# Optimization experiments

Measured on AMD Instinct MI355X. Metric: run time of the kernel, lower is better.

The kernel has to match this reference:

```python
import jax, jax.numpy as jnp
import numpy as np
from jax import lax

D_MODEL, D_STATE, D_CONV, EXPAND = 512, 16, 4, 2
D_INNER = EXPAND * D_MODEL          # 1024
DT_RANK = (D_MODEL + 15) // 16      # 32
BATCH, SEQ = 4, 1024


def setup_inputs() -> dict:
    key = jax.random.key(0)
    ks = jax.random.split(key, 8)
    s = 0.02
    x = jax.random.normal(ks[0], (BATCH, SEQ, D_MODEL), jnp.float32)
    in_proj_w = jax.random.normal(ks[1], (2 * D_INNER, D_MODEL), jnp.float32) * s
    conv_w = jax.random.normal(ks[2], (D_INNER, 1, D_CONV), jnp.float32) * s  # depthwise
    conv_b = jnp.zeros((D_INNER,), jnp.float32)
    x_proj_w = jax.random.normal(ks[3], (DT_RANK + 2 * D_STATE, D_INNER), jnp.float32) * s
    dt_proj_w = jax.random.normal(ks[4], (D_INNER, DT_RANK), jnp.float32) * s
    dt_proj_b = jax.random.normal(ks[5], (D_INNER,), jnp.float32) * 0.1
    # Mamba S4D-real init: A = -[1..d_state] per channel, stored as log
    A_log = jnp.log(jnp.tile(jnp.arange(1, D_STATE + 1, dtype=jnp.float32)[None, :], (D_INNER, 1)))
    D = jnp.ones((D_INNER,), jnp.float32)
    out_proj_w = jax.random.normal(ks[6], (D_MODEL, D_INNER), jnp.float32) * s
    ln_w = jnp.ones((D_MODEL,), jnp.float32)
    ln_b = jnp.zeros((D_MODEL,), jnp.float32)
    return dict(x=x, in_proj_w=in_proj_w, conv_w=conv_w, conv_b=conv_b,
                x_proj_w=x_proj_w, dt_proj_w=dt_proj_w, dt_proj_b=dt_proj_b,
                A_log=A_log, D=D, out_proj_w=out_proj_w, ln_w=ln_w, ln_b=ln_b)


def _selective_scan(u, delta, A, Bm, Cm, D):
    # u, delta: (B,L,Di); A: (Di,N); Bm, Cm: (B,L,N)
    dA = jnp.exp(delta[..., None] * A)                    # (B,L,Di,N)
    dBu = (delta * u)[..., None] * Bm[:, :, None, :]      # (B,L,Di,N)
    dA_t = jnp.moveaxis(dA, 1, 0)                         # (L,B,Di,N)
    dBu_t = jnp.moveaxis(dBu, 1, 0)
    C_t = jnp.moveaxis(Cm, 1, 0)                          # (L,B,N)

    def step(h, inp):
        dA_i, dBu_i, C_i = inp
        h = dA_i * h + dBu_i                              # (B,Di,N)
        y = jnp.einsum('bdn,bn->bd', h, C_i)
        return h, y

    h0 = jnp.zeros((u.shape[0], A.shape[0], A.shape[1]), u.dtype)
    _, ys = lax.scan(step, h0, (dA_t, dBu_t, C_t))        # ys: (L,B,Di)
    return jnp.moveaxis(ys, 0, 1) + u * D                 # (B,L,Di)


def reference(x, in_proj_w, conv_w, conv_b, x_proj_w, dt_proj_w, dt_proj_b,
              A_log, D, out_proj_w, ln_w, ln_b):
    # ---- Mamba SSM ----
    xz = jnp.einsum('bld,ed->ble', x, in_proj_w)          # (B,L,2*Di)
    xs, z = jnp.split(xz, 2, axis=-1)
    # causal depthwise conv over time
    xt = jnp.moveaxis(xs, 1, 2)                           # (B,Di,L)
    xt = lax.conv_general_dilated(xt, conv_w, window_strides=(1,),
                                  padding=[(D_CONV - 1, 0)],
                                  feature_group_count=D_INNER,
                                  dimension_numbers=('NCH', 'OIH', 'NCH'))
    xt = xt + conv_b[None, :, None]
    u = jax.nn.silu(jnp.moveaxis(xt, 1, 2))               # (B,L,Di)

    x_dbl = jnp.einsum('bld,ed->ble', u, x_proj_w)        # (B,L,dt_rank+2N)
    dt = x_dbl[..., :DT_RANK]
    Bm = x_dbl[..., DT_RANK:DT_RANK + D_STATE]
    Cm = x_dbl[..., DT_RANK + D_STATE:]
    delta = jax.nn.softplus(jnp.einsum('blr,dr->bld', dt, dt_proj_w) + dt_proj_b)
    A = -jnp.exp(A_log)                                   # (Di,N)

    y = _selective_scan(u, delta, A, Bm, Cm, D)
    y = y * jax.nn.silu(z)
    ssm_out = jnp.einsum('ble,de->bld', y, out_proj_w)    # (B,L,Dm)

    # ---- residual + LayerNorm ----
    r = x + ssm_out
    mu = jnp.mean(r, axis=-1, keepdims=True)
    var = jnp.mean(jnp.square(r - mu), axis=-1, keepdims=True)
    return (r - mu) / jnp.sqrt(var + 1e-5) * ln_w + ln_b
```

## Files before the change

kernel.cpp:

```cpp
#include <hip/hip_runtime.h>
#include <hip/hip_bf16.h>
#include <math.h>

#define B_   4
#define L_   1024
#define DM   512
#define DI   1024
#define NS   16
#define XDC  64
#define BL   4096
#define G_   16
#define SEG  64
#define KS   4

typedef short bfrag __attribute__((ext_vector_type(8)));
typedef float ffrag __attribute__((ext_vector_type(4)));

__device__ __forceinline__ ushort f2bf(float v) {
    __hip_bfloat16 h = __float2bfloat16(v);
    return *(ushort*)&h;
}

__global__ __launch_bounds__(256) void cast_bf16(const float* __restrict__ in,
        ushort* __restrict__ out, int n4)
{
    int i = blockIdx.x * 256 + threadIdx.x;
    if (i >= n4) return;
    float4 v = ((const float4*)in)[i];
    ushort4 o;
    o.x = f2bf(v.x); o.y = f2bf(v.y); o.z = f2bf(v.z); o.w = f2bf(v.w);
    ((ushort4*)out)[i] = o;
}

template<int EPI>
__global__ __launch_bounds__(256) void gemm_mfma(const ushort* __restrict__ A,
        const ushort* __restrict__ B, float* __restrict__ C,
        int K, int ldc, const float* __restrict__ resid)
{
    __shared__ ushort As[128][40];
    __shared__ ushort Bs[128][40];
    const int tid = threadIdx.x;
    const int lane = tid & 63, wave = tid >> 6;
    const int wm = (wave & 1) * 64, wn = (wave >> 1) * 64;
    const int l15 = lane & 15, quad = lane >> 4;
    const int m0 = blockIdx.y * 128, n0 = blockIdx.x * 128;

    ffrag acc[4][4] = {};

    for (int k0 = 0; k0 < K; k0 += 32) {
        #pragma unroll
        for (int i = 0; i < 2; i++) {
            int chunk = tid + i * 256;
            int row = chunk >> 2, kk8 = (chunk & 3) * 8;
            *(uint4*)&As[row][kk8] = *(const uint4*)&A[(size_t)(m0 + row) * K + k0 + kk8];
            *(uint4*)&Bs[row][kk8] = *(const uint4*)&B[(size_t)(n0 + row) * K + k0 + kk8];
        }
        __syncthreads();
        bfrag af[4], bfv[4];
        #pragma unroll
        for (int i = 0; i < 4; i++) {
            af[i]  = *(const bfrag*)&As[wm + i * 16 + l15][quad * 8];
            bfv[i] = *(const bfrag*)&Bs[wn + i * 16 + l15][quad * 8];
        }
        #pragma unroll
        for (int i = 0; i < 4; i++)
            #pragma unroll
            for (int j = 0; j < 4; j++)
                acc[i][j] = __builtin_amdgcn_mfma_f32_16x16x32_bf16(af[i], bfv[j], acc[i][j], 0, 0, 0);
        __syncthreads();
    }

    #pragma unroll
    for (int i = 0; i < 4; i++) {
        #pragma unroll
        for (int j = 0; j < 4; j++) {
            int n = n0 + wn + j * 16 + l15;
            #pragma unroll
            for (int r = 0; r < 4; r++) {
                int m = m0 + wm + i * 16 + quad * 4 + r;
                float v = acc[i][j][r];
                if (EPI == 2) v += resid[(size_t)m * ldc + n];
                C[(size_t)m * ldc + n] = v;
            }
        }
    }
}

__global__ __launch_bounds__(256) void gemm_tn128(const float* __restrict__ A,
        const float* __restrict__ W, float* __restrict__ C,
        int N, int K, int lda, int ldw, int ldc,
        const float* __restrict__ bias)
{
    __shared__ float As[16][132];
    __shared__ float Ws[16][68];
    const int tid = threadIdx.x;
    const int tx = tid & 15, ty = tid >> 4;
    const int n0 = blockIdx.x * 64, m0 = blockIdx.y * 128;
    float acc[8][4] = {};

    for (int k0 = 0; k0 < K; k0 += 16) {
        #pragma unroll
        for (int i = 0; i < 2; i++) {
            int idx = tid * 2 + i;
            int r = idx >> 2, c4 = (idx & 3) * 4;
            const float4 v = *(const float4*)&A[(size_t)(m0 + r) * lda + k0 + c4];
            As[c4 + 0][r] = v.x; As[c4 + 1][r] = v.y;
            As[c4 + 2][r] = v.z; As[c4 + 3][r] = v.w;
        }
        {
            int r = tid >> 2, c4 = (tid & 3) * 4;
            const float4 v = *(const float4*)&W[(size_t)(n0 + r) * ldw + k0 + c4];
            Ws[c4 + 0][r] = v.x; Ws[c4 + 1][r] = v.y;
            Ws[c4 + 2][r] = v.z; Ws[c4 + 3][r] = v.w;
        }
        __syncthreads();
        #pragma unroll
        for (int kk = 0; kk < 16; kk++) {
            float a[8], b[4];
            #pragma unroll
            for (int i = 0; i < 8; i++) a[i] = As[kk][ty * 8 + i];
            #pragma unroll
            for (int j = 0; j < 4; j++) b[j] = Ws[kk][tx * 4 + j];
            #pragma unroll
            for (int i = 0; i < 8; i++)
                #pragma unroll
                for (int j = 0; j < 4; j++)
                    acc[i][j] = fmaf(a[i], b[j], acc[i][j]);
        }
        __syncthreads();
    }

    #pragma unroll
    for (int i = 0; i < 8; i++) {
        int m = m0 + ty * 8 + i;
        int nb = n0 + tx * 4;
        float4 v = make_float4(acc[i][0], acc[i][1], acc[i][2], acc[i][3]);
        float bm = bias[m];
        v.x += bm; v.y += bm; v.z += bm; v.w += bm;
        v.x = (v.x > 20.f) ? v.x : log1pf(__expf(v.x));
        v.y = (v.y > 20.f) ? v.y : log1pf(__expf(v.y));
        v.z = (v.z > 20.f) ? v.z : log1pf(__expf(v.z));
        v.w = (v.w > 20.f) ? v.w : log1pf(__expf(v.w));
        *(float4*)&C[(size_t)m * ldc + nb] = v;
    }
}

__global__ __launch_bounds__(256) void gemm3_splitk(const float* __restrict__ uT,
        const float* __restrict__ xw, float* __restrict__ part)
{
    __shared__ float As[16][33];
    __shared__ float Ws[16][68];
    const int tid = threadIdx.x;
    const int tx = tid & 15, ty = tid >> 4;
    const int ks = blockIdx.x, m0 = blockIdx.y * 32;
    const int kbase = ks * (DI / KS);
    float acc[2][4] = {};

    for (int k0 = 0; k0 < DI / KS; k0 += 16) {
        if (tid < 128) {
            int k = tid >> 3, m4 = (tid & 7) * 4;
            const float4 v = *(const float4*)&uT[(size_t)(kbase + k0 + k) * BL + m0 + m4];
            As[k][m4 + 0] = v.x; As[k][m4 + 1] = v.y;
            As[k][m4 + 2] = v.z; As[k][m4 + 3] = v.w;
        }
        {
            int r = tid >> 2, c4 = (tid & 3) * 4;
            const float4 v = *(const float4*)&xw[(size_t)r * DI + kbase + k0 + c4];
            Ws[c4 + 0][r] = v.x; Ws[c4 + 1][r] = v.y;
            Ws[c4 + 2][r] = v.z; Ws[c4 + 3][r] = v.w;
        }
        __syncthreads();
        #pragma unroll
        for (int kk = 0; kk < 16; kk++) {
            float a[2], b[4];
            a[0] = As[kk][ty * 2 + 0];
            a[1] = As[kk][ty * 2 + 1];
            #pragma unroll
            for (int j = 0; j < 4; j++) b[j] = Ws[kk][tx * 4 + j];
            #pragma unroll
            for (int i = 0; i < 2; i++)
                #pragma unroll
                for (int j = 0; j < 4; j++)
                    acc[i][j] = fmaf(a[i], b[j], acc[i][j]);
        }
        __syncthreads();
    }

    float* pp = part + (size_t)ks * BL * XDC;
    #pragma unroll
    for (int i = 0; i < 2; i++) {
        int m = m0 + ty * 2 + i;
        *(float4*)&pp[(size_t)m * XDC + tx * 4] =
            make_float4(acc[i][0], acc[i][1], acc[i][2], acc[i][3]);
    }
}

__global__ __launch_bounds__(256) void gemm3_reduce(const float* __restrict__ part,
        float* __restrict__ xdbl)
{
    int i = blockIdx.x * 256 + threadIdx.x;
    const float4* p0 = (const float4*)part;
    float4 a = p0[i];
    #pragma unroll
    for (int s = 1; s < KS; s++) {
        float4 b = p0[i + (size_t)s * BL * XDC / 4];
        a.x += b.x; a.y += b.y; a.z += b.z; a.w += b.w;
    }
    ((float4*)xdbl)[i] = a;
}

__global__ __launch_bounds__(256) void conv_silu(const float* __restrict__ xzT,
        const float* __restrict__ cw, const float* __restrict__ cb,
        float* __restrict__ uT)
{
    int i = blockIdx.x * 256 + threadIdx.x;
    int d  = i >> 10;
    int q  = i & 1023;
    int bl = q * 4;
    int l  = bl & (L_ - 1);
    const float* row = xzT + (size_t)d * BL;
    float4 cur = *(const float4*)&row[bl];
    float4 prev = make_float4(0.f, 0.f, 0.f, 0.f);
    if (l != 0) prev = *(const float4*)&row[bl - 4];
    float v[7] = { prev.y, prev.z, prev.w, cur.x, cur.y, cur.z, cur.w };
    float w0 = cw[d * 4 + 0], w1 = cw[d * 4 + 1], w2 = cw[d * 4 + 2], w3 = cw[d * 4 + 3];
    float bias = cb[d];
    float4 o;
    o.x = bias + w0 * v[0] + w1 * v[1] + w2 * v[2] + w3 * v[3];
    o.y = bias + w0 * v[1] + w1 * v[2] + w2 * v[3] + w3 * v[4];
    o.z = bias + w0 * v[2] + w1 * v[3] + w2 * v[4] + w3 * v[5];
    o.w = bias + w0 * v[3] + w1 * v[4] + w2 * v[5] + w3 * v[6];
    o.x = o.x / (1.f + __expf(-o.x));
    o.y = o.y / (1.f + __expf(-o.y));
    o.z = o.z / (1.f + __expf(-o.z));
    o.w = o.w / (1.f + __expf(-o.w));
    *(float4*)&uT[(size_t)d * BL + bl] = o;
}

__global__ __launch_bounds__(256) void scan_part1(const float* __restrict__ deltaT,
        const float* __restrict__ uT, const float* __restrict__ xdbl,
        const float* __restrict__ A_log, float* __restrict__ h_end,
        float* __restrict__ Sdv)
{
    const int t = blockIdx.x * 256 + threadIdx.x;
    const int n = t & 15;
    const int seg = (t >> 4) & (G_ - 1);
    const int d = (t >> 8) & (DI - 1);
    const int b = t >> 18;

    const float Acoef = -__expf(A_log[d * NS + n]);
    float h = 0.f, sdv = 0.f;

    const size_t base_t = (size_t)d * BL + b * L_ + seg * SEG;
    const size_t base_x = (size_t)b * L_ * XDC + (size_t)seg * SEG * XDC;

    for (int l0 = 0; l0 < SEG; l0 += 16) {
        float dv[16], uv[16], Bv[16];
        {
            const float4* dp = (const float4*)(deltaT + base_t + l0);
            const float4* up = (const float4*)(uT + base_t + l0);
            #pragma unroll
            for (int i = 0; i < 4; i++) {
                *(float4*)&dv[i * 4] = dp[i];
                *(float4*)&uv[i * 4] = up[i];
            }
        }
        {
            const float* xp = xdbl + base_x + (size_t)l0 * XDC + 32 + n;
            #pragma unroll
            for (int j = 0; j < 16; j++) Bv[j] = xp[j * XDC];
        }
        #pragma unroll
        for (int j = 0; j < 16; j++) {
            sdv += dv[j];
            Bv[j] *= dv[j] * uv[j];
            dv[j] = __expf(dv[j] * Acoef);
        }
        #pragma unroll
        for (int j = 0; j < 16; j++)
            h = fmaf(dv[j], h, Bv[j]);
    }
    const int si = ((b * DI + d) * G_ + seg);
    h_end[si * NS + n] = h;
    if (n == 0) Sdv[si] = sdv;
}

__global__ __launch_bounds__(256) void scan_part2(const float* __restrict__ h_end,
        const float* __restrict__ Sdv, const float* __restrict__ A_log,
        float* __restrict__ h0)
{
    const int t = blockIdx.x * 256 + threadIdx.x;
    const int n = t & 15;
    const int g = t >> 4;
    const int d = g & (DI - 1);
    const float Acoef = -__expf(A_log[d * NS + n]);
    float H = 0.f;
    #pragma unroll
    for (int s = 0; s < G_; s++) {
        const int si = g * G_ + s;
        h0[si * NS + n] = H;
        H = h_end[si * NS + n] + __expf(Acoef * Sdv[si]) * H;
    }
}

__global__ __launch_bounds__(256) void scan_part3(const float* __restrict__ deltaT,
        const float* __restrict__ uT, const float* __restrict__ xdbl,
        const float* __restrict__ xzT, const float* __restrict__ A_log,
        const float* __restrict__ Dp, const float* __restrict__ h0,
        float* __restrict__ yT)
{
    const int t = blockIdx.x * 256 + threadIdx.x;
    const int n = t & 15;
    const int seg = (t >> 4) & (G_ - 1);
    const int d = (t >> 8) & (DI - 1);
    const int b = t >> 18;

    const float Acoef = -__expf(A_log[d * NS + n]);
    const float Dd = Dp[d];
    float h = h0[((b * DI + d) * G_ + seg) * NS + n];

    const size_t base_t = (size_t)d * BL + b * L_ + seg * SEG;
    const size_t base_z = (size_t)(DI + d) * BL + b * L_ + seg * SEG;
    const size_t base_x = (size_t)b * L_ * XDC + (size_t)seg * SEG * XDC;

    for (int l0 = 0; l0 < SEG; l0 += 16) {
        float ug = uT [base_t + l0 + n];
        float zg = xzT[base_z + l0 + n];

        float dv[16], uv[16];
        {
            const float4* dp = (const float4*)(deltaT + base_t + l0);
            const float4* up = (const float4*)(uT + base_t + l0);
            #pragma unroll
            for (int i = 0; i < 4; i++) {
                *(float4*)&dv[i * 4] = dp[i];
                *(float4*)&uv[i * 4] = up[i];
            }
        }
        float Bv[16], Cv[16];
        {
            const float* xp = xdbl + base_x + (size_t)l0 * XDC + 32 + n;
            #pragma unroll
            for (int j = 0; j < 16; j++) {
                Bv[j] = xp[j * XDC];
                Cv[j] = xp[j * XDC + 16];
            }
        }
        #pragma unroll
        for (int j = 0; j < 16; j++) {
            Bv[j] *= dv[j] * uv[j];
            dv[j] = __expf(dv[j] * Acoef);
        }
        float p[16];
        #pragma unroll
        for (int j = 0; j < 16; j++) {
            h = fmaf(dv[j], h, Bv[j]);
            p[j] = h * Cv[j];
        }

        float q8[8];
        #pragma unroll
        for (int k = 0; k < 8; k++) {
            float tt = (n & 8) ? p[k] : p[k + 8];
            float rr = __shfl_xor(tt, 8);
            q8[k] = ((n & 8) ? p[k + 8] : p[k]) + rr;
        }
        float q4[4];
        #pragma unroll
        for (int k = 0; k < 4; k++) {
            float tt = (n & 4) ? q8[k] : q8[k + 4];
            float rr = __shfl_xor(tt, 4);
            q4[k] = ((n & 4) ? q8[k + 4] : q8[k]) + rr;
        }
        float q2[2];
        #pragma unroll
        for (int k = 0; k < 2; k++) {
            float tt = (n & 2) ? q4[k] : q4[k + 2];
            float rr = __shfl_xor(tt, 2);
            q2[k] = ((n & 2) ? q4[k + 2] : q4[k]) + rr;
        }
        float tt = (n & 1) ? q2[0] : q2[1];
        float rr = __shfl_xor(tt, 1);
        float S = ((n & 1) ? q2[1] : q2[0]) + rr;

        float v = S + ug * Dd;
        v *= zg / (1.f + __expf(-zg));
        yT[base_t + l0 + n] = v;
    }
}

__global__ __launch_bounds__(256) void transpose_cast(const float* __restrict__ yT,
        ushort* __restrict__ yB)
{
    __shared__ float t[64][65];
    const int bl0 = blockIdx.x * 64, d0 = blockIdx.y * 64;
    const int tid = threadIdx.x;
    #pragma unroll
    for (int i = 0; i < 4; i++) {
        int chunk = tid + i * 256;
        int dr = chunk >> 4, c4 = (chunk & 15) * 4;
        const float4 v = *(const float4*)&yT[(size_t)(d0 + dr) * BL + bl0 + c4];
        t[dr][c4 + 0] = v.x; t[dr][c4 + 1] = v.y;
        t[dr][c4 + 2] = v.z; t[dr][c4 + 3] = v.w;
    }
    __syncthreads();
    #pragma unroll
    for (int i = 0; i < 4; i++) {
        int chunk = tid + i * 256;
        int br = chunk >> 4, dc4 = (chunk & 15) * 4;
        ushort4 o;
        o.x = f2bf(t[dc4 + 0][br]); o.y = f2bf(t[dc4 + 1][br]);
        o.z = f2bf(t[dc4 + 2][br]); o.w = f2bf(t[dc4 + 3][br]);
        *(ushort4*)&yB[(size_t)(bl0 + br) * DI + d0 + dc4] = o;
    }
}

__global__ __launch_bounds__(256) void ln_kernel(const float* __restrict__ r,
        const float* __restrict__ lnw, const float* __restrict__ lnb,
        float* __restrict__ out)
{
    int row = blockIdx.x;
    const float* rr = r + (size_t)row * DM;
    float v0 = rr[threadIdx.x], v1 = rr[threadIdx.x + 256];
    float s = v0 + v1, s2 = v0 * v0 + v1 * v1;
    #pragma unroll
    for (int off = 32; off > 0; off >>= 1) {
        s  += __shfl_down(s, off);
        s2 += __shfl_down(s2, off);
    }
    __shared__ float ls[4], ls2[4];
    __shared__ float mu_s, rstd_s;
    int wid = threadIdx.x >> 6, lane = threadIdx.x & 63;
    if (lane == 0) { ls[wid] = s; ls2[wid] = s2; }
    __syncthreads();
    if (threadIdx.x == 0) {
        float S = ls[0] + ls[1] + ls[2] + ls[3];
        float S2 = ls2[0] + ls2[1] + ls2[2] + ls2[3];
        float mu = S * (1.f / DM);
        float var = S2 * (1.f / DM) - mu * mu;
        mu_s = mu;
        rstd_s = rsqrtf(var + 1e-5f);
    }
    __syncthreads();
    float mu = mu_s, rstd = rstd_s;
    out[(size_t)row * DM + threadIdx.x] =
        (v0 - mu) * rstd * lnw[threadIdx.x] + lnb[threadIdx.x];
    out[(size_t)row * DM + threadIdx.x + 256] =
        (v1 - mu) * rstd * lnw[threadIdx.x + 256] + lnb[threadIdx.x + 256];
}

extern "C" void kernel_launch(void* const* d_in, const int* in_sizes, int n_in,
                              void* d_out, int out_size, void* d_ws, size_t ws_size,
                              hipStream_t stream)
{
    const float* x         = (const float*)d_in[0];
    const float* in_proj_w = (const float*)d_in[1];
    const float* conv_w    = (const float*)d_in[2];
    const float* conv_b    = (const float*)d_in[3];
    const float* x_proj_w  = (const float*)d_in[4];
    const float* dt_proj_w = (const float*)d_in[5];
    const float* dt_proj_b = (const float*)d_in[6];
    const float* A_log     = (const float*)d_in[7];
    const float* Dvec      = (const float*)d_in[8];
    const float* out_proj_w= (const float*)d_in[9];
    const float* ln_w      = (const float*)d_in[10];
    const float* ln_b      = (const float*)d_in[11];
    float* out = (float*)d_out;

    float* ws     = (float*)d_ws;
    float* xzT    = ws;
    float* uT     = xzT    + (size_t)2048 * BL;
    float* xdbl   = uT     + (size_t)DI * BL;
    float* deltaT = xdbl   + (size_t)BL * XDC;
    float* yT     = deltaT + (size_t)DI * BL;
    float* r      = yT     + (size_t)DI * BL;
    ushort* xB    = (ushort*)yT;
    float*  xdblp = yT;
    float*  Sdv   = yT + (size_t)KS * BL * XDC;
    ushort* yB    = (ushort*)deltaT;
    ushort* wOutB = (ushort*)deltaT + (size_t)4 * 1024 * 1024;
    ushort* wInB  = (ushort*)deltaT + (size_t)9 * 1024 * 1024 / 2;
    float* h_end  = r;
    float* h0     = r + (size_t)B_ * DI * G_ * NS;

    dim3 blk(256);

    cast_bf16<<<(BL * DM / 4 + 255) / 256, blk, 0, stream>>>(x, xB, BL * DM / 4);
    cast_bf16<<<(2048 * DM / 4 + 255) / 256, blk, 0, stream>>>(in_proj_w, wInB, 2048 * DM / 4);

    gemm_mfma<0><<<dim3(BL / 128, 2048 / 128), blk, 0, stream>>>(
        wInB, xB, xzT, DM, BL, nullptr);

    conv_silu<<<(DI * BL / 4) / 256, blk, 0, stream>>>(xzT, conv_w, conv_b, uT);

    gemm3_splitk<<<dim3(KS, BL / 32), blk, 0, stream>>>(uT, x_proj_w, xdblp);
    gemm3_reduce<<<(BL * XDC / 4) / 256, blk, 0, stream>>>(xdblp, xdbl);

    gemm_tn128<<<dim3(BL / 64, DI / 128), blk, 0, stream>>>(
        dt_proj_w, xdbl, deltaT, BL, 32, 32, XDC, BL, dt_proj_b);

    scan_part1<<<(B_ * DI * G_ * NS) / 256, blk, 0, stream>>>(
        deltaT, uT, xdbl, A_log, h_end, Sdv);
    scan_part2<<<(B_ * DI * NS) / 256, blk, 0, stream>>>(
        h_end, Sdv, A_log, h0);
    scan_part3<<<(B_ * DI * G_ * NS) / 256, blk, 0, stream>>>(
        deltaT, uT, xdbl, xzT, A_log, Dvec, h0, yT);

    transpose_cast<<<dim3(BL / 64, DI / 64), blk, 0, stream>>>(yT, yB);
    cast_bf16<<<(DM * DI / 4 + 255) / 256, blk, 0, stream>>>(out_proj_w, wOutB, DM * DI / 4);

    gemm_mfma<2><<<dim3(DM / 128, BL / 128), blk, 0, stream>>>(
        yB, wOutB, r, DI, DM, x);

    ln_kernel<<<BL, blk, 0, stream>>>(r, ln_w, ln_b, out);
}
```

Before: 271.1 us.

## Fuse three-pass chunked scan into one kernel and move dt_proj to bf16 MFMA

The three scan kernels (per-segment partial scan, cross-segment carry, final scan) are merged into one kernel where each block owns one (batch, channel) pair. Segment end states and carries are exchanged through shared memory, which removes two launches and the global round trips for h_end, Sdv and h0. The fp32 SIMT dt_proj GEMM is replaced by the bf16 MFMA GEMM with a bias-plus-softplus epilogue. The bf16 dt input is produced inside the split-K reduce and a cast of dt_proj_w is added. The cost is lower precision in delta and a serial 16-step carry loop run by one wave per block.

```diff
diff --git a/kernel.cpp b/kernel.cpp
--- a/kernel.cpp
+++ b/kernel.cpp
@@ -35,7 +35,8 @@
 template<int EPI>
 __global__ __launch_bounds__(256) void gemm_mfma(const ushort* __restrict__ A,
         const ushort* __restrict__ B, float* __restrict__ C,
-        int K, int ldc, const float* __restrict__ resid)
+        int K, int ldc, const float* __restrict__ resid,
+        const float* __restrict__ bias)
 {
     __shared__ ushort As[128][40];
     __shared__ ushort Bs[128][40];
@@ -80,68 +81,13 @@
                 int m = m0 + wm + i * 16 + quad * 4 + r;
                 float v = acc[i][j][r];
                 if (EPI == 2) v += resid[(size_t)m * ldc + n];
+                if (EPI == 3) {
+                    v += bias[m];
+                    v = (v > 20.f) ? v : log1pf(__expf(v));
+                }
                 C[(size_t)m * ldc + n] = v;
             }
         }
-    }
-}
-
-__global__ __launch_bounds__(256) void gemm_tn128(const float* __restrict__ A,
-        const float* __restrict__ W, float* __restrict__ C,
-        int N, int K, int lda, int ldw, int ldc,
-        const float* __restrict__ bias)
-{
-    __shared__ float As[16][132];
-    __shared__ float Ws[16][68];
-    const int tid = threadIdx.x;
-    const int tx = tid & 15, ty = tid >> 4;
-    const int n0 = blockIdx.x * 64, m0 = blockIdx.y * 128;
-    float acc[8][4] = {};
-
-    for (int k0 = 0; k0 < K; k0 += 16) {
-        #pragma unroll
-        for (int i = 0; i < 2; i++) {
-            int idx = tid * 2 + i;
-            int r = idx >> 2, c4 = (idx & 3) * 4;
-            const float4 v = *(const float4*)&A[(size_t)(m0 + r) * lda + k0 + c4];
-            As[c4 + 0][r] = v.x; As[c4 + 1][r] = v.y;
-            As[c4 + 2][r] = v.z; As[c4 + 3][r] = v.w;
-        }
-        {
-            int r = tid >> 2, c4 = (tid & 3) * 4;
-            const float4 v = *(const float4*)&W[(size_t)(n0 + r) * ldw + k0 + c4];
-            Ws[c4 + 0][r] = v.x; Ws[c4 + 1][r] = v.y;
-            Ws[c4 + 2][r] = v.z; Ws[c4 + 3][r] = v.w;
-        }
-        __syncthreads();
-        #pragma unroll
-        for (int kk = 0; kk < 16; kk++) {
-            float a[8], b[4];
-            #pragma unroll
-            for (int i = 0; i < 8; i++) a[i] = As[kk][ty * 8 + i];
-            #pragma unroll
-            for (int j = 0; j < 4; j++) b[j] = Ws[kk][tx * 4 + j];
-            #pragma unroll
-            for (int i = 0; i < 8; i++)
-                #pragma unroll
-                for (int j = 0; j < 4; j++)
-                    acc[i][j] = fmaf(a[i], b[j], acc[i][j]);
-        }
-        __syncthreads();
-    }
-
-    #pragma unroll
-    for (int i = 0; i < 8; i++) {
-        int m = m0 + ty * 8 + i;
-        int nb = n0 + tx * 4;
-        float4 v = make_float4(acc[i][0], acc[i][1], acc[i][2], acc[i][3]);
-        float bm = bias[m];
-        v.x += bm; v.y += bm; v.z += bm; v.w += bm;
-        v.x = (v.x > 20.f) ? v.x : log1pf(__expf(v.x));
-        v.y = (v.y > 20.f) ? v.y : log1pf(__expf(v.y));
-        v.z = (v.z > 20.f) ? v.z : log1pf(__expf(v.z));
-        v.w = (v.w > 20.f) ? v.w : log1pf(__expf(v.w));
-        *(float4*)&C[(size_t)m * ldc + nb] = v;
     }
 }
 
@@ -196,7 +142,7 @@
 }
 
 __global__ __launch_bounds__(256) void gemm3_reduce(const float* __restrict__ part,
-        float* __restrict__ xdbl)
+        float* __restrict__ xdbl, ushort* __restrict__ dtB)
 {
     int i = blockIdx.x * 256 + threadIdx.x;
     const float4* p0 = (const float4*)part;
@@ -207,6 +153,13 @@
         a.x += b.x; a.y += b.y; a.z += b.z; a.w += b.w;
     }
     ((float4*)xdbl)[i] = a;
+    int c4 = i & 15;
+    if (c4 < 8) {
+        int m = i >> 4;
+        ushort4 o;
+        o.x = f2bf(a.x); o.y = f2bf(a.y); o.z = f2bf(a.z); o.w = f2bf(a.w);
+        ((ushort4*)dtB)[m * 8 + c4] = o;
+    }
 }
 
 __global__ __launch_bounds__(256) void conv_silu(const float* __restrict__ xzT,
@@ -237,23 +190,30 @@
     *(float4*)&uT[(size_t)d * BL + bl] = o;
 }
 
-__global__ __launch_bounds__(256) void scan_part1(const float* __restrict__ deltaT,
+__global__ __launch_bounds__(256) void scan_fused(const float* __restrict__ deltaT,
         const float* __restrict__ uT, const float* __restrict__ xdbl,
-        const float* __restrict__ A_log, float* __restrict__ h_end,
-        float* __restrict__ Sdv)
-{
-    const int t = blockIdx.x * 256 + threadIdx.x;
-    const int n = t & 15;
-    const int seg = (t >> 4) & (G_ - 1);
-    const int d = (t >> 8) & (DI - 1);
-    const int b = t >> 18;
+        const float* __restrict__ xzT, const float* __restrict__ A_log,
+        const float* __restrict__ Dp, float* __restrict__ yT)
+{
+    __shared__ float hend_s[G_][NS + 1];
+    __shared__ float h0_s[G_][NS + 1];
+    __shared__ float sdv_s[G_];
+
+    const int tid = threadIdx.x;
+    const int n = tid & 15;
+    const int seg = tid >> 4;
+    const int bd = blockIdx.x;
+    const int d = bd & (DI - 1);
+    const int b = bd >> 10;
 
     const float Acoef = -__expf(A_log[d * NS + n]);
+    const float Dd = Dp[d];
+
+    const size_t base_t = (size_t)d * BL + b * L_ + seg * SEG;
+    const size_t base_z = (size_t)(DI + d) * BL + b * L_ + seg * SEG;
+    const size_t base_x = (size_t)b * L_ * XDC + (size_t)seg * SEG * XDC;
+
     float h = 0.f, sdv = 0.f;
-
-    const size_t base_t = (size_t)d * BL + b * L_ + seg * SEG;
-    const size_t base_x = (size_t)b * L_ * XDC + (size_t)seg * SEG * XDC;
-
     for (int l0 = 0; l0 < SEG; l0 += 16) {
         float dv[16], uv[16], Bv[16];
         {
@@ -280,49 +240,21 @@
         for (int j = 0; j < 16; j++)
             h = fmaf(dv[j], h, Bv[j]);
     }
-    const int si = ((b * DI + d) * G_ + seg);
-    h_end[si * NS + n] = h;
-    if (n == 0) Sdv[si] = sdv;
-}
-
-__global__ __launch_bounds__(256) void scan_part2(const float* __restrict__ h_end,
-        const float* __restrict__ Sdv, const float* __restrict__ A_log,
-        float* __restrict__ h0)
-{
-    const int t = blockIdx.x * 256 + threadIdx.x;
-    const int n = t & 15;
-    const int g = t >> 4;
-    const int d = g & (DI - 1);
-    const float Acoef = -__expf(A_log[d * NS + n]);
-    float H = 0.f;
-    #pragma unroll
-    for (int s = 0; s < G_; s++) {
-        const int si = g * G_ + s;
-        h0[si * NS + n] = H;
-        H = h_end[si * NS + n] + __expf(Acoef * Sdv[si]) * H;
-    }
-}
-
-__global__ __launch_bounds__(256) void scan_part3(const float* __restrict__ deltaT,
-        const float* __restrict__ uT, const float* __restrict__ xdbl,
-        const float* __restrict__ xzT, const float* __restrict__ A_log,
-        const float* __restrict__ Dp, const float* __restrict__ h0,
-        float* __restrict__ yT)
-{
-    const int t = blockIdx.x * 256 + threadIdx.x;
-    const int n = t & 15;
-    const int seg = (t >> 4) & (G_ - 1);
-    const int d = (t >> 8) & (DI - 1);
-    const int b = t >> 18;
-
-    const float Acoef = -__expf(A_log[d * NS + n]);
-    const float Dd = Dp[d];
-    float h = h0[((b * DI + d) * G_ + seg) * NS + n];
-
-    const size_t base_t = (size_t)d * BL + b * L_ + seg * SEG;
-    const size_t base_z = (size_t)(DI + d) * BL + b * L_ + seg * SEG;
-    const size_t base_x = (size_t)b * L_ * XDC + (size_t)seg * SEG * XDC;
-
+    hend_s[seg][n] = h;
+    if (n == 0) sdv_s[seg] = sdv;
+    __syncthreads();
+
+    if (seg == 0) {
+        float H = 0.f;
+        #pragma unroll
+        for (int s = 0; s < G_; s++) {
+            h0_s[s][n] = H;
+            H = hend_s[s][n] + __expf(Acoef * sdv_s[s]) * H;
+        }
+    }
+    __syncthreads();
+
+    h = h0_s[seg][n];
     for (int l0 = 0; l0 < SEG; l0 += 16) {
         float ug = uT [base_t + l0 + n];
         float zg = xzT[base_z + l0 + n];
@@ -476,41 +408,37 @@
     float* r      = yT     + (size_t)DI * BL;
     ushort* xB    = (ushort*)yT;
     float*  xdblp = yT;
-    float*  Sdv   = yT + (size_t)KS * BL * XDC;
     ushort* yB    = (ushort*)deltaT;
     ushort* wOutB = (ushort*)deltaT + (size_t)4 * 1024 * 1024;
     ushort* wInB  = (ushort*)deltaT + (size_t)9 * 1024 * 1024 / 2;
-    float* h_end  = r;
-    float* h0     = r + (size_t)B_ * DI * G_ * NS;
+    ushort* dtB   = (ushort*)r;
+    ushort* dtwB  = (ushort*)r + (size_t)BL * 32;
 
     dim3 blk(256);
 
     cast_bf16<<<(BL * DM / 4 + 255) / 256, blk, 0, stream>>>(x, xB, BL * DM / 4);
     cast_bf16<<<(2048 * DM / 4 + 255) / 256, blk, 0, stream>>>(in_proj_w, wInB, 2048 * DM / 4);
+    cast_bf16<<<(DI * 32 / 4 + 255) / 256, blk, 0, stream>>>(dt_proj_w, dtwB, DI * 32 / 4);
 
     gemm_mfma<0><<<dim3(BL / 128, 2048 / 128), blk, 0, stream>>>(
-        wInB, xB, xzT, DM, BL, nullptr);
+        wInB, xB, xzT, DM, BL, nullptr, nullptr);
 
     conv_silu<<<(DI * BL / 4) / 256, blk, 0, stream>>>(xzT, conv_w, conv_b, uT);
 
     gemm3_splitk<<<dim3(KS, BL / 32), blk, 0, stream>>>(uT, x_proj_w, xdblp);
-    gemm3_reduce<<<(BL * XDC / 4) / 256, blk, 0, stream>>>(xdblp, xdbl);
-
-    gemm_tn128<<<dim3(BL / 64, DI / 128), blk, 0, stream>>>(
-        dt_proj_w, xdbl, deltaT, BL, 32, 32, XDC, BL, dt_proj_b);
-
-    scan_part1<<<(B_ * DI * G_ * NS) / 256, blk, 0, stream>>>(
-        deltaT, uT, xdbl, A_log, h_end, Sdv);
-    scan_part2<<<(B_ * DI * NS) / 256, blk, 0, stream>>>(
-        h_end, Sdv, A_log, h0);
-    scan_part3<<<(B_ * DI * G_ * NS) / 256, blk, 0, stream>>>(
-        deltaT, uT, xdbl, xzT, A_log, Dvec, h0, yT);
+    gemm3_reduce<<<(BL * XDC / 4) / 256, blk, 0, stream>>>(xdblp, xdbl, dtB);
+
+    gemm_mfma<3><<<dim3(BL / 128, DI / 128), blk, 0, stream>>>(
+        dtwB, dtB, deltaT, 32, BL, nullptr, dt_proj_b);
+
+    scan_fused<<<B_ * DI, blk, 0, stream>>>(
+        deltaT, uT, xdbl, xzT, A_log, Dvec, yT);
 
     transpose_cast<<<dim3(BL / 64, DI / 64), blk, 0, stream>>>(yT, yB);
     cast_bf16<<<(DM * DI / 4 + 255) / 256, blk, 0, stream>>>(out_proj_w, wOutB, DM * DI / 4);
 
     gemm_mfma<2><<<dim3(DM / 128, BL / 128), blk, 0, stream>>>(
-        yB, wOutB, r, DI, DM, x);
+        yB, wOutB, r, DI, DM, x, nullptr);
 
     ln_kernel<<<BL, blk, 0, stream>>>(r, ln_w, ln_b, out);
 }
```

After: 269.5 us. Within noise of the previous version (-0.6%).
